# Optimization experiments

Measured on AMD Instinct MI355X. Metric: run time of the kernel, lower is better.

## Reference

```python
import jax, jax.numpy as jnp
import numpy as np
from jax import lax

# Model dims (mamba_ssm defaults: d_state=16, d_conv=4, expand=2, dt_rank=ceil(d_model/16))
V = 16384       # vocab_size
D = 1024        # embedding_dim / d_model
C_CLS = 128     # num_CLS_classes
D_INNER = 2 * D # expand * d_model = 2048
N = 16          # d_state
K = 4           # d_conv
DT_RANK = (D + 15) // 16  # 64
B, L = 4, 512


def setup_inputs() -> dict:
    key = jax.random.key(0)
    ks = jax.random.split(key, 12)
    s = 0.02
    tokens = jax.random.randint(ks[0], (B, L), 0, V, dtype=jnp.int64)
    embedding = jax.random.normal(ks[1], (V, D), jnp.float32) * s
    in_proj_w = jax.random.normal(ks[2], (2 * D_INNER, D), jnp.float32) * s
    conv_w = jax.random.normal(ks[3], (D_INNER, 1, K), jnp.float32) * 0.1
    conv_b = jnp.zeros((D_INNER,), jnp.float32)
    x_proj_w = jax.random.normal(ks[4], (DT_RANK + 2 * N, D_INNER), jnp.float32) * s
    dt_proj_w = jax.random.normal(ks[5], (D_INNER, DT_RANK), jnp.float32) * s
    dt_proj_b = jax.random.uniform(ks[6], (D_INNER,), jnp.float32, -4.0, -2.0)  # softplus -> small dt
    A_log = jnp.log(jnp.broadcast_to(jnp.arange(1, N + 1, dtype=jnp.float32), (D_INNER, N)))
    D_param = jnp.ones((D_INNER,), jnp.float32)
    out_proj_w = jax.random.normal(ks[7], (D, D_INNER), jnp.float32) * s
    recon_w = jax.random.normal(ks[8], (V, D), jnp.float32) * s
    cls_w = jax.random.normal(ks[9], (C_CLS, D), jnp.float32) * s
    return dict(tokens=tokens, embedding=embedding, in_proj_w=in_proj_w,
                conv_w=conv_w, conv_b=conv_b, x_proj_w=x_proj_w,
                dt_proj_w=dt_proj_w, dt_proj_b=dt_proj_b, A_log=A_log,
                D_param=D_param, out_proj_w=out_proj_w, recon_w=recon_w, cls_w=cls_w)


def _mamba(h, in_proj_w, conv_w, conv_b, x_proj_w, dt_proj_w, dt_proj_b, A_log, D_param, out_proj_w):
    # h: (B, L, D)
    xz = jnp.einsum('bld,ed->ble', h, in_proj_w)          # (B, L, 2*D_INNER)
    x, z = jnp.split(xz, 2, axis=-1)                      # each (B, L, D_INNER)
    # causal depthwise conv1d along L
    xt = jnp.swapaxes(x, 1, 2)                            # (B, D_INNER, L)
    xt = lax.conv_general_dilated(xt, conv_w, window_strides=(1,),
                                  padding=[(K - 1, 0)],
                                  feature_group_count=D_INNER,
                                  dimension_numbers=('NCH', 'OIH', 'NCH'))
    xt = xt + conv_b[None, :, None]
    x = jax.nn.silu(jnp.swapaxes(xt, 1, 2))               # (B, L, D_INNER)
    # input-dependent dt, B, C
    x_dbl = jnp.einsum('bld,ed->ble', x, x_proj_w)        # (B, L, DT_RANK+2N)
    dt, Bm, Cm = jnp.split(x_dbl, [DT_RANK, DT_RANK + N], axis=-1)
    delta = jax.nn.softplus(jnp.einsum('blr,dr->bld', dt, dt_proj_w) + dt_proj_b)  # (B,L,D_INNER)
    A = -jnp.exp(A_log)                                   # (D_INNER, N)
    dA = jnp.exp(delta[..., None] * A)                    # (B,L,D_INNER,N)
    dBx = delta[..., None] * Bm[:, :, None, :] * x[..., None]  # (B,L,D_INNER,N)
    # selective scan over time (sequential recurrence)
    dA_t = jnp.swapaxes(dA, 0, 1)                         # (L,B,D_INNER,N)
    dBx_t = jnp.swapaxes(dBx, 0, 1)
    C_t = jnp.swapaxes(Cm, 0, 1)                          # (L,B,N)
    def step(hc, inp):
        a, bx, c = inp
        hc = a * hc + bx                                  # (B,D_INNER,N)
        y = jnp.einsum('bdn,bn->bd', hc, c)
        return hc, y
    h0 = jnp.zeros((x.shape[0], D_INNER, N), x.dtype)
    _, ys = lax.scan(step, h0, (dA_t, dBx_t, C_t))
    y = jnp.swapaxes(ys, 0, 1) + x * D_param              # (B,L,D_INNER)
    y = y * jax.nn.silu(z)
    return jnp.einsum('ble,de->bld', y, out_proj_w)       # (B,L,D)


def reference(tokens, embedding, in_proj_w, conv_w, conv_b, x_proj_w,
              dt_proj_w, dt_proj_b, A_log, D_param, out_proj_w, recon_w, cls_w):
    h = embedding[tokens]                                 # (B,L,D)
    h = _mamba(h, in_proj_w, conv_w, conv_b, x_proj_w, dt_proj_w, dt_proj_b,
               A_log, D_param, out_proj_w)
    recon = jnp.einsum('bld,vd->blv', h, recon_w)         # (B,L,V)
    pooled = h.mean(axis=1)                               # mean CLS pooling assumption
    cls = jnp.einsum('bd,cd->bc', pooled, cls_w)          # (B,C_CLS)
    return (recon, cls)
```

## Files before the change

### kernel.cpp

```cpp
#include <hip/hip_runtime.h>
#include <hip/hip_bf16.h>
#include <stdint.h>

#define DIN    2048
#define MROWS  2048
#define LSEQ   512
#define NV     16384
#define DMODEL 1024
#define NC     8
#define CL     64

typedef __attribute__((ext_vector_type(8))) short bf16x8;
typedef __attribute__((ext_vector_type(4))) float f32x4;

__device__ __forceinline__ uint16_t f2bf(float f) {
  uint32_t u = __builtin_bit_cast(uint32_t, f);
  u += 0x7fffu + ((u >> 16) & 1u);
  return (uint16_t)(u >> 16);
}
__device__ __forceinline__ float bf2f(uint16_t u) {
  return __builtin_bit_cast(float, (uint32_t)u << 16);
}

__device__ __forceinline__ void gld_lds16(const uint16_t* g, uint16_t* l) {
  __builtin_amdgcn_global_load_lds(
      (const __attribute__((address_space(1))) void*)g,
      (__attribute__((address_space(3))) void*)l,
      16, 0, 0);
}

__global__ __launch_bounds__(512, 2) void gemm256_bf16_kernel(
    const uint16_t* __restrict__ A, const uint16_t* __restrict__ B,
    float* __restrict__ Cf, uint16_t* __restrict__ Cbf, int M, int N, int K)
{
  __shared__ uint16_t lds[4 * 16384];
  const int tid = threadIdx.x;
  const int w   = tid >> 6;
  const int l   = tid & 63;

  const int nwg = gridDim.x;
  const int cpx = nwg >> 3;
  const int swz = (blockIdx.x & 7) * cpx + (blockIdx.x >> 3);
  const int nmy = M >> 8;
  const int bm  = (swz % nmy) << 8;
  const int bn  = (swz / nmy) << 8;

  const int fr = l & 15;
  const int fg = l >> 4;
  const int wr = w >> 2;
  const int wc = w & 3;

  const int srow = l >> 2;
  const int kof  = (((l & 3) ^ ((l >> 3) & 3)) << 3);
  const int ar0  = (w * 2 + 0) * 16 + srow;
  const int ar1  = (w * 2 + 1) * 16 + srow;
  const uint16_t* Ag0 = A + (size_t)(bm + ar0) * K + kof;
  const uint16_t* Ag1 = A + (size_t)(bm + ar1) * K + kof;
  const uint16_t* Bg0 = B + (size_t)(bn + ar0) * K + kof;
  const uint16_t* Bg1 = B + (size_t)(bn + ar1) * K + kof;
  const int lA0 = (w * 2 + 0) * 512;
  const int lA1 = (w * 2 + 1) * 512;
  const int lB0 = 8192 + (w * 2 + 0) * 512;
  const int lB1 = 8192 + (w * 2 + 1) * 512;

  const int axr  = ((fg ^ ((fr >> 1) & 3)) << 3);
  const int aoff = (wr * 128 + fr) * 32 + axr;
  const int boff = 8192 + (wc * 64 + fr) * 32 + axr;

  f32x4 acc[8][4] = {};
  const int NT = K >> 5;

  auto stage_all = [&](int t) {
    const int sb = (t & 3) << 14;
    const int k0 = t << 5;
    gld_lds16(Ag0 + k0, lds + sb + lA0);
    gld_lds16(Ag1 + k0, lds + sb + lA1);
    gld_lds16(Bg0 + k0, lds + sb + lB0);
    gld_lds16(Bg1 + k0, lds + sb + lB1);
  };
  auto compute_full = [&](int sb) {
    bf16x8 af[8], bfr[4];
#pragma unroll
    for (int mi = 0; mi < 8; ++mi)
      af[mi] = *(const bf16x8*)(lds + sb + aoff + mi * 512);
#pragma unroll
    for (int ni = 0; ni < 4; ++ni)
      bfr[ni] = *(const bf16x8*)(lds + sb + boff + ni * 512);
    __builtin_amdgcn_s_setprio(1);
#pragma unroll
    for (int mi = 0; mi < 8; ++mi)
#pragma unroll
      for (int ni = 0; ni < 4; ++ni)
        acc[mi][ni] = __builtin_amdgcn_mfma_f32_16x16x32_bf16(af[mi], bfr[ni], acc[mi][ni], 0, 0, 0);
    __builtin_amdgcn_s_setprio(0);
  };

  stage_all(0); stage_all(1); stage_all(2);
  asm volatile("s_waitcnt vmcnt(8)" ::: "memory");
  __builtin_amdgcn_s_barrier();

  for (int t = 0; t < NT - 3; ++t) {
    const int sb = (t & 3) << 14;
    const int st = ((t + 3) & 3) << 14;
    const int k0 = (t + 3) << 5;
    bf16x8 af[8], bfr[4];
#pragma unroll
    for (int mi = 0; mi < 8; ++mi)
      af[mi] = *(const bf16x8*)(lds + sb + aoff + mi * 512);
    bfr[0] = *(const bf16x8*)(lds + sb + boff + 0 * 512);
    bfr[1] = *(const bf16x8*)(lds + sb + boff + 1 * 512);
    gld_lds16(Ag0 + k0, lds + st + lA0);
    gld_lds16(Ag1 + k0, lds + st + lA1);
    __builtin_amdgcn_s_barrier();
    asm volatile("s_waitcnt lgkmcnt(0)" ::: "memory");
    __builtin_amdgcn_sched_barrier(0);
    __builtin_amdgcn_s_setprio(1);
#pragma unroll
    for (int mi = 0; mi < 8; ++mi)
#pragma unroll
      for (int ni = 0; ni < 2; ++ni)
        acc[mi][ni] = __builtin_amdgcn_mfma_f32_16x16x32_bf16(af[mi], bfr[ni], acc[mi][ni], 0, 0, 0);
    __builtin_amdgcn_s_setprio(0);
    __builtin_amdgcn_s_barrier();
    bfr[2] = *(const bf16x8*)(lds + sb + boff + 2 * 512);
    bfr[3] = *(const bf16x8*)(lds + sb + boff + 3 * 512);
    gld_lds16(Bg0 + k0, lds + st + lB0);
    gld_lds16(Bg1 + k0, lds + st + lB1);
    __builtin_amdgcn_s_barrier();
    asm volatile("s_waitcnt lgkmcnt(0)" ::: "memory");
    __builtin_amdgcn_sched_barrier(0);
    __builtin_amdgcn_s_setprio(1);
#pragma unroll
    for (int mi = 0; mi < 8; ++mi)
#pragma unroll
      for (int ni = 2; ni < 4; ++ni)
        acc[mi][ni] = __builtin_amdgcn_mfma_f32_16x16x32_bf16(af[mi], bfr[ni], acc[mi][ni], 0, 0, 0);
    __builtin_amdgcn_s_setprio(0);
    asm volatile("s_waitcnt vmcnt(8)" ::: "memory");
    __builtin_amdgcn_s_barrier();
  }
  compute_full(((NT - 3) & 3) << 14);
  asm volatile("s_waitcnt vmcnt(4)" ::: "memory");
  __builtin_amdgcn_s_barrier();
  compute_full(((NT - 2) & 3) << 14);
  asm volatile("s_waitcnt vmcnt(0)" ::: "memory");
  __builtin_amdgcn_s_barrier();
  compute_full(((NT - 1) & 3) << 14);

#pragma unroll
  for (int mi = 0; mi < 8; ++mi) {
    const int r0 = bm + wr * 128 + mi * 16 + fg * 4;
#pragma unroll
    for (int ni = 0; ni < 4; ++ni) {
      const int c0 = bn + wc * 64 + ni * 16 + fr;
#pragma unroll
      for (int r = 0; r < 4; ++r) {
        const float v = acc[mi][ni][r];
        if (Cf)  Cf[(size_t)(r0 + r) * N + c0] = v;
        if (Cbf) Cbf[(size_t)(r0 + r) * N + c0] = f2bf(v);
      }
    }
  }
}

__global__ __launch_bounds__(256) void gemm_bf16_kernel(
    const uint16_t* __restrict__ A, const uint16_t* __restrict__ B,
    float* __restrict__ C, int M, int N, int K, int kchunk,
    const float* __restrict__ bias)
{
  __shared__ uint16_t As[128 * 32];
  __shared__ uint16_t Bs[128 * 32];
  const int tid  = threadIdx.x;
  const int wid  = tid >> 6;
  const int lane = tid & 63;
  const int bm = blockIdx.y * 128;
  const int bn = blockIdx.x * 128;
  const int k_beg = blockIdx.z * kchunk;
  float* Cout = C + (size_t)blockIdx.z * M * N;

  const int fr = lane & 15;
  const int fg = lane >> 4;
  const int wm = (wid >> 1) * 64;
  const int wn = (wid & 1) * 64;

  const int srow = wid * 32 + (lane >> 2);
  const int skof = (lane & 3) * 8;
  const uint16_t* Ag = A + (size_t)(bm + srow) * K + skof;
  const uint16_t* Bg = B + (size_t)(bn + srow) * K + skof;
  uint16_t* Al = As + wid * 1024;
  uint16_t* Bl = Bs + wid * 1024;

  f32x4 acc[4][4] = {};

  for (int k0 = 0; k0 < kchunk; k0 += 32) {
    const int kk = k_beg + k0;
    gld_lds16(Ag + kk, Al);
    gld_lds16(Ag + (size_t)16 * K + kk, Al + 512);
    gld_lds16(Bg + kk, Bl);
    gld_lds16(Bg + (size_t)16 * K + kk, Bl + 512);
    asm volatile("s_waitcnt vmcnt(0)" ::: "memory");
    __syncthreads();
    bf16x8 af[4], bfr[4];
#pragma unroll
    for (int i = 0; i < 4; ++i)
      af[i] = *(const bf16x8*)(As + (wm + i * 16 + fr) * 32 + fg * 8);
#pragma unroll
    for (int j = 0; j < 4; ++j)
      bfr[j] = *(const bf16x8*)(Bs + (wn + j * 16 + fr) * 32 + fg * 8);
#pragma unroll
    for (int i = 0; i < 4; ++i)
#pragma unroll
      for (int j = 0; j < 4; ++j)
        acc[i][j] = __builtin_amdgcn_mfma_f32_16x16x32_bf16(af[i], bfr[j], acc[i][j], 0, 0, 0);
    __syncthreads();
  }

#pragma unroll
  for (int i = 0; i < 4; ++i) {
    const int r0 = bm + wm + i * 16 + fg * 4;
#pragma unroll
    for (int j = 0; j < 4; ++j) {
      const int c0 = bn + wn + j * 16 + fr;
      const float bv = bias ? bias[c0] : 0.f;
#pragma unroll
      for (int r = 0; r < 4; ++r) {
        float v = acc[i][j][r];
        if (bias) {
          const float u = v + bv;
          v = (u > 20.f) ? u : log1pf(__expf(u));
        }
        Cout[(size_t)(r0 + r) * N + c0] = v;
      }
    }
  }
}

__global__ __launch_bounds__(256) void reduce4_dt_kernel(
    const float* __restrict__ in, float* __restrict__ xdbl, uint16_t* __restrict__ dtb) {
  const int i = blockIdx.x * 256 + threadIdx.x;
  const float s = in[i] + in[i + 262144] + in[i + 2 * 262144] + in[i + 3 * 262144];
  xdbl[i] = s;
  const int c = i & 127;
  if (c < 64) dtb[(i >> 7) * 64 + c] = f2bf(s);
}

__global__ __launch_bounds__(256) void reduce2_bf16_kernel(
    const float* __restrict__ in, uint16_t* __restrict__ outb, int n) {
  const int i = blockIdx.x * 256 + threadIdx.x;
  if (i >= n) return;
  outb[i] = f2bf(in[i] + in[i + (size_t)n]);
}

__global__ __launch_bounds__(256) void embed_kernel(
    const int* __restrict__ tok, const float* __restrict__ emb, uint16_t* __restrict__ out) {
  const int m = blockIdx.x;
  const int t = tok[m];
  const float4 v = ((const float4*)(emb + (size_t)t * DMODEL))[threadIdx.x];
  ((ushort4*)(out + (size_t)m * DMODEL))[threadIdx.x] =
      make_ushort4(f2bf(v.x), f2bf(v.y), f2bf(v.z), f2bf(v.w));
}

__global__ __launch_bounds__(256) void cvt_bf16_kernel(
    const float* __restrict__ in, uint16_t* __restrict__ out, int n4) {
  const int i = blockIdx.x * 256 + threadIdx.x;
  if (i >= n4) return;
  const float4 v = ((const float4*)in)[i];
  ((ushort4*)out)[i] = make_ushort4(f2bf(v.x), f2bf(v.y), f2bf(v.z), f2bf(v.w));
}

__global__ __launch_bounds__(256) void cvt_pad_kernel(
    const float* __restrict__ in, uint16_t* __restrict__ out, int rows_in, int cols4) {
  const int i = blockIdx.x * 256 + threadIdx.x;
  const int r = i / cols4, c = i % cols4;
  ushort4 o = make_ushort4(0, 0, 0, 0);
  if (r < rows_in) {
    const float4 v = ((const float4*)in)[(size_t)r * cols4 + c];
    o = make_ushort4(f2bf(v.x), f2bf(v.y), f2bf(v.z), f2bf(v.w));
  }
  ((ushort4*)out)[i] = o;
}

__global__ __launch_bounds__(256) void conv_silu_kernel(
    const float* __restrict__ xz, const float* __restrict__ cw, const float* __restrict__ cb,
    float* __restrict__ xc, uint16_t* __restrict__ xcb)
{
  const int idx = blockIdx.x * 256 + threadIdx.x;
  const int d = idx & (DIN - 1);
  const int m = idx >> 11;
  const int l = m & (LSEQ - 1);
  float acc = cb[d];
#pragma unroll
  for (int j = 0; j < 4; ++j) {
    const int lj = l - 3 + j;
    if (lj >= 0) acc += cw[d * 4 + j] * xz[(size_t)(m - 3 + j) * 4096 + d];
  }
  const float r = acc / (1.f + __expf(-acc));
  xc[idx] = r;
  xcb[idx] = f2bf(r);
}

__global__ __launch_bounds__(256) void scan_partial_kernel(
    const float* __restrict__ delta, const float* __restrict__ xc,
    const float* __restrict__ xdbl, const float* __restrict__ A_log,
    float* __restrict__ Pb, float* __restrict__ Qb)
{
  const int q = threadIdx.x & 3;
  const int d_idx = threadIdx.x >> 2;
  const int c = blockIdx.x;
  const int d = blockIdx.y * 64 + d_idx;
  const int b = blockIdx.z;
  float Arow[4];
#pragma unroll
  for (int n = 0; n < 4; ++n)
    Arow[n] = -expf(A_log[d * 16 + q * 4 + n]);
  float P[4] = {1.f, 1.f, 1.f, 1.f};
  float Q[4] = {0.f, 0.f, 0.f, 0.f};
  const int l0 = c * CL;
#pragma unroll 4
  for (int li = 0; li < CL; ++li) {
    const int m = b * LSEQ + l0 + li;
    const float de = delta[(size_t)m * DIN + d];
    const float xv = xc[(size_t)m * DIN + d];
    const float dx = de * xv;
    const float4 Bv = *(const float4*)(xdbl + (size_t)m * 128 + 64 + q * 4);
    const float bv[4] = {Bv.x, Bv.y, Bv.z, Bv.w};
#pragma unroll
    for (int n = 0; n < 4; ++n) {
      const float a = __expf(de * Arow[n]);
      P[n] *= a;
      Q[n] = a * Q[n] + dx * bv[n];
    }
  }
  const size_t o = ((size_t)(b * NC + c) * DIN + d) * 16 + q * 4;
  *(float4*)(Pb + o) = make_float4(P[0], P[1], P[2], P[3]);
  *(float4*)(Qb + o) = make_float4(Q[0], Q[1], Q[2], Q[3]);
}

__global__ __launch_bounds__(256) void scan_bounds_kernel(
    const float* __restrict__ Pb, const float* __restrict__ Qb, float* __restrict__ Hi)
{
  const int i = blockIdx.x * 256 + threadIdx.x;
  const int b = i >> 15;
  const int r = i & 32767;
  float h = 0.f;
#pragma unroll
  for (int c = 0; c < NC; ++c) {
    const size_t o = ((size_t)(b * NC + c) << 15) + r;
    Hi[o] = h;
    h = Pb[o] * h + Qb[o];
  }
}

__global__ __launch_bounds__(256) void scan_final_kernel(
    const float* __restrict__ delta, const float* __restrict__ xc,
    const float* __restrict__ xdbl, const float* __restrict__ xz,
    const float* __restrict__ A_log, const float* __restrict__ Dp,
    const float* __restrict__ Hi, uint16_t* __restrict__ yb)
{
  const int q = threadIdx.x & 3;
  const int d_idx = threadIdx.x >> 2;
  const int c = blockIdx.x;
  const int d = blockIdx.y * 64 + d_idx;
  const int b = blockIdx.z;
  float Arow[4];
#pragma unroll
  for (int n = 0; n < 4; ++n)
    Arow[n] = -expf(A_log[d * 16 + q * 4 + n]);
  const float dpd = Dp[d];
  const size_t o = ((size_t)(b * NC + c) * DIN + d) * 16 + q * 4;
  const float4 Hv = *(const float4*)(Hi + o);
  float h[4] = {Hv.x, Hv.y, Hv.z, Hv.w};
  const int l0 = c * CL;
#pragma unroll 2
  for (int li = 0; li < CL; ++li) {
    const int m = b * LSEQ + l0 + li;
    const float de = delta[(size_t)m * DIN + d];
    const float xv = xc[(size_t)m * DIN + d];
    const float dx = de * xv;
    const float4 Bv = *(const float4*)(xdbl + (size_t)m * 128 + 64 + q * 4);
    const float4 Cv = *(const float4*)(xdbl + (size_t)m * 128 + 80 + q * 4);
    const float bv[4] = {Bv.x, Bv.y, Bv.z, Bv.w};
    const float cv[4] = {Cv.x, Cv.y, Cv.z, Cv.w};
    float yp = 0.f;
#pragma unroll
    for (int n = 0; n < 4; ++n) {
      const float a = __expf(de * Arow[n]);
      h[n] = a * h[n] + dx * bv[n];
      yp += h[n] * cv[n];
    }
    yp += __shfl_xor(yp, 1);
    yp += __shfl_xor(yp, 2);
    if (q == 0) {
      const float z = xz[(size_t)m * 4096 + 2048 + d];
      const float sil = z / (1.f + __expf(-z));
      yb[(size_t)m * DIN + d] = f2bf((yp + xv * dpd) * sil);
    }
  }
}

__global__ __launch_bounds__(256) void pool1_kernel(
    const uint16_t* __restrict__ h2b, float* __restrict__ part) {
  const int b = blockIdx.x >> 4, s = blockIdx.x & 15;
  const int c = threadIdx.x * 4;
  const uint16_t* base = h2b + ((size_t)(b * LSEQ + s * 32)) * DMODEL + c;
  float a0 = 0, a1 = 0, a2 = 0, a3 = 0;
  for (int l = 0; l < 32; ++l) {
    const ushort4 v = *(const ushort4*)(base + (size_t)l * DMODEL);
    a0 += bf2f(v.x); a1 += bf2f(v.y); a2 += bf2f(v.z); a3 += bf2f(v.w);
  }
  *(float4*)(part + (size_t)blockIdx.x * DMODEL + c) = make_float4(a0, a1, a2, a3);
}

__global__ __launch_bounds__(256) void pool2_cls_kernel(
    const float* __restrict__ part, const float* __restrict__ w, float* __restrict__ out) {
  __shared__ float pl[DMODEL];
  const int b = blockIdx.x, t = threadIdx.x;
  float4 s = make_float4(0, 0, 0, 0);
  for (int k = 0; k < 16; ++k) {
    const float4 v = *(const float4*)(part + ((size_t)(b * 16 + k)) * DMODEL + t * 4);
    s.x += v.x; s.y += v.y; s.z += v.z; s.w += v.w;
  }
  const float inv = 1.f / (float)LSEQ;
  pl[t * 4 + 0] = s.x * inv; pl[t * 4 + 1] = s.y * inv;
  pl[t * 4 + 2] = s.z * inv; pl[t * 4 + 3] = s.w * inv;
  __syncthreads();
  if (t < 128) {
    const float* wr = w + (size_t)t * DMODEL;
    float acc = 0.f;
    for (int k = 0; k < DMODEL; ++k) acc += pl[k] * wr[k];
    out[b * 128 + t] = acc;
  }
}

extern "C" void kernel_launch(void* const* d_in, const int* in_sizes, int n_in,
                              void* d_out, int out_size, void* d_ws, size_t ws_size,
                              hipStream_t stream) {
  const int*   tokens    = (const int*)d_in[0];
  const float* embedding = (const float*)d_in[1];
  const float* in_proj_w = (const float*)d_in[2];
  const float* conv_w    = (const float*)d_in[3];
  const float* conv_b    = (const float*)d_in[4];
  const float* x_proj_w  = (const float*)d_in[5];
  const float* dt_proj_w = (const float*)d_in[6];
  const float* dt_proj_b = (const float*)d_in[7];
  const float* A_log     = (const float*)d_in[8];
  const float* D_param   = (const float*)d_in[9];
  const float* out_prj_w = (const float*)d_in[10];
  const float* recon_w   = (const float*)d_in[11];
  const float* cls_w     = (const float*)d_in[12];

  char* ws = (char*)d_ws;
  const size_t MB = 1024 * 1024;
  uint16_t* h_bf   = (uint16_t*)(ws + 0);
  uint16_t* w_in   = (uint16_t*)(ws + 4 * MB);
  float*    xz     = (float*)(ws + 12 * MB);
  float*    xc_f   = (float*)(ws + 44 * MB);
  uint16_t* xc_b   = (uint16_t*)(ws + 60 * MB);
  uint16_t* wx_bf  = (uint16_t*)(ws + 68 * MB);
  float*    xdbl   = (float*)(ws + 69 * MB);
  uint16_t* dt_bf  = (uint16_t*)(ws + 70 * MB);
  uint16_t* wdt_bf = (uint16_t*)(ws + 71 * MB);
  float*    delta  = (float*)(ws + 72 * MB);
  uint16_t* y_bf   = (uint16_t*)(ws + 88 * MB);
  uint16_t* h2_bf  = (uint16_t*)(ws + 96 * MB);
  float*    part   = (float*)(ws + 100 * MB);
  uint16_t* wout_bf = h_bf;
  uint16_t* wrec_bf = (uint16_t*)xz;
  float*    kscr    = delta;
  float*    Pbuf    = (float*)(ws + 60 * MB);
  float*    Qbuf    = (float*)(ws + 64 * MB);
  float*    Hinit   = (float*)(ws + 4 * MB);

  const int RECON = MROWS * NV;

  embed_kernel<<<dim3(MROWS), dim3(256), 0, stream>>>(tokens, embedding, h_bf);
  cvt_bf16_kernel<<<dim3(4096), dim3(256), 0, stream>>>(in_proj_w, w_in, 4096 * 1024 / 4);
  gemm256_bf16_kernel<<<dim3(128), dim3(512), 0, stream>>>(h_bf, w_in, xz, nullptr, MROWS, 4096, 1024);
  cvt_bf16_kernel<<<dim3(2048), dim3(256), 0, stream>>>(out_prj_w, wout_bf, 1024 * 2048 / 4);
  cvt_bf16_kernel<<<dim3(128), dim3(256), 0, stream>>>(dt_proj_w, wdt_bf, 2048 * 64 / 4);
  cvt_pad_kernel<<<dim3(256), dim3(256), 0, stream>>>(x_proj_w, wx_bf, 96, 512);
  conv_silu_kernel<<<dim3(16384), dim3(256), 0, stream>>>(xz, conv_w, conv_b, xc_f, xc_b);
  gemm_bf16_kernel<<<dim3(1, 16, 4), dim3(256), 0, stream>>>(xc_b, wx_bf, kscr, MROWS, 128, 2048, 512, nullptr);
  reduce4_dt_kernel<<<dim3(1024), dim3(256), 0, stream>>>(kscr, xdbl, dt_bf);
  gemm_bf16_kernel<<<dim3(16, 16, 1), dim3(256), 0, stream>>>(dt_bf, wdt_bf, delta, MROWS, DIN, 64, 64, dt_proj_b);
  scan_partial_kernel<<<dim3(NC, 32, 4), dim3(256), 0, stream>>>(delta, xc_f, xdbl, A_log, Pbuf, Qbuf);
  scan_bounds_kernel<<<dim3(512), dim3(256), 0, stream>>>(Pbuf, Qbuf, Hinit);
  scan_final_kernel<<<dim3(NC, 32, 4), dim3(256), 0, stream>>>(delta, xc_f, xdbl, xz, A_log, D_param, Hinit, y_bf);
  cvt_bf16_kernel<<<dim3(16384), dim3(256), 0, stream>>>(recon_w, wrec_bf, NV * 1024 / 4);
  gemm_bf16_kernel<<<dim3(8, 16, 2), dim3(256), 0, stream>>>(y_bf, wout_bf, kscr, MROWS, 1024, 2048, 1024, nullptr);
  reduce2_bf16_kernel<<<dim3(8192), dim3(256), 0, stream>>>(kscr, h2_bf, MROWS * 1024);
  gemm256_bf16_kernel<<<dim3(512), dim3(512), 0, stream>>>(h2_bf, wrec_bf, (float*)d_out, nullptr, MROWS, NV, 1024);
  pool1_kernel<<<dim3(64), dim3(256), 0, stream>>>(h2_bf, part);
  pool2_cls_kernel<<<dim3(4), dim3(256), 0, stream>>>(part, cls_w, (float*)d_out + RECON);
}
```

Measured before the change: 375.0 us.

## Rewrite 256x256 GEMM with BK=64 double-buffered 8-phase pipelined schedule

Replaces the four-stage BK=32 pipeline of the large bf16 GEMM with a two-buffer BK=64 scheme. Each K-tile is split into eight MFMA phases interleaved with LDS reads and global-to-LDS loads, using a new XOR swizzle for 128-byte rows. The aim is fewer barriers per unit of work and better overlap of loads with MFMA. The unused bf16 output path is dropped. The more complex phase schedule with many barriers risks stalls or occupancy changes.

```diff
diff --git a/kernel.cpp b/kernel.cpp
--- a/kernel.cpp
+++ b/kernel.cpp
@@ -29,11 +29,11 @@
       16, 0, 0);
 }
 
-__global__ __launch_bounds__(512, 2) void gemm256_bf16_kernel(
+__global__ __launch_bounds__(512, 2) void gemm256p8_kernel(
     const uint16_t* __restrict__ A, const uint16_t* __restrict__ B,
-    float* __restrict__ Cf, uint16_t* __restrict__ Cbf, int M, int N, int K)
-{
-  __shared__ uint16_t lds[4 * 16384];
+    float* __restrict__ C, int M, int N, int K)
+{
+  __shared__ uint16_t lds[2 * 32768];
   const int tid = threadIdx.x;
   const int w   = tid >> 6;
   const int l   = tid & 63;
@@ -50,102 +50,108 @@
   const int wr = w >> 2;
   const int wc = w & 3;
 
-  const int srow = l >> 2;
-  const int kof  = (((l & 3) ^ ((l >> 3) & 3)) << 3);
-  const int ar0  = (w * 2 + 0) * 16 + srow;
-  const int ar1  = (w * 2 + 1) * 16 + srow;
-  const uint16_t* Ag0 = A + (size_t)(bm + ar0) * K + kof;
-  const uint16_t* Ag1 = A + (size_t)(bm + ar1) * K + kof;
-  const uint16_t* Bg0 = B + (size_t)(bn + ar0) * K + kof;
-  const uint16_t* Bg1 = B + (size_t)(bn + ar1) * K + kof;
-  const int lA0 = (w * 2 + 0) * 512;
-  const int lA1 = (w * 2 + 1) * 512;
-  const int lB0 = 8192 + (w * 2 + 0) * 512;
-  const int lB1 = 8192 + (w * 2 + 1) * 512;
-
-  const int axr  = ((fg ^ ((fr >> 1) & 3)) << 3);
-  const int aoff = (wr * 128 + fr) * 32 + axr;
-  const int boff = 8192 + (wc * 64 + fr) * 32 + axr;
+  const int schunk = (l & 7) ^ (l >> 3);
+  const uint16_t* Ag = A + (size_t)(bm + w * 16 + (l >> 3)) * K + schunk * 8;
+  const uint16_t* Bg = B + (size_t)(bn + w * 16 + (l >> 3)) * K + schunk * 8;
+
+  const int ax0 = ((fg) ^ (fr & 7)) << 3;
+  const int ax1 = ((4 + fg) ^ (fr & 7)) << 3;
+  const int aA  = (wr * 128 + fr) * 64;
+  const int aB  = 16384 + (wc * 64 + fr) * 64;
 
   f32x4 acc[8][4] = {};
-  const int NT = K >> 5;
-
-  auto stage_all = [&](int t) {
-    const int sb = (t & 3) << 14;
-    const int k0 = t << 5;
-    gld_lds16(Ag0 + k0, lds + sb + lA0);
-    gld_lds16(Ag1 + k0, lds + sb + lA1);
-    gld_lds16(Bg0 + k0, lds + sb + lB0);
-    gld_lds16(Bg1 + k0, lds + sb + lB1);
+  bf16x8 af[4][2], b01[2][2], b23[2][2];
+
+  const int NT = K >> 6;
+  const int NITER = NT >> 1;
+
+  auto STG = [&](int t, int h) {
+    const uint16_t* g = ((h & 2) ? Bg : Ag) + ((h & 1) ? (size_t)128 * K : 0) + (size_t)t * 64;
+    uint16_t* d = lds + ((t & 1) << 15) + ((h & 2) << 13) + (((h & 1) << 7) + (w << 4)) * 64;
+    gld_lds16(g, d);
+    gld_lds16(g + (size_t)8 * K, d + 512);
   };
-  auto compute_full = [&](int sb) {
-    bf16x8 af[8], bfr[4];
-#pragma unroll
-    for (int mi = 0; mi < 8; ++mi)
-      af[mi] = *(const bf16x8*)(lds + sb + aoff + mi * 512);
-#pragma unroll
-    for (int ni = 0; ni < 4; ++ni)
-      bfr[ni] = *(const bf16x8*)(lds + sb + boff + ni * 512);
-    __builtin_amdgcn_s_setprio(1);
-#pragma unroll
-    for (int mi = 0; mi < 8; ++mi)
-#pragma unroll
-      for (int ni = 0; ni < 4; ++ni)
-        acc[mi][ni] = __builtin_amdgcn_mfma_f32_16x16x32_bf16(af[mi], bfr[ni], acc[mi][ni], 0, 0, 0);
-    __builtin_amdgcn_s_setprio(0);
-  };
-
-  stage_all(0); stage_all(1); stage_all(2);
-  asm volatile("s_waitcnt vmcnt(8)" ::: "memory");
-  __builtin_amdgcn_s_barrier();
-
-  for (int t = 0; t < NT - 3; ++t) {
-    const int sb = (t & 3) << 14;
-    const int st = ((t + 3) & 3) << 14;
-    const int k0 = (t + 3) << 5;
-    bf16x8 af[8], bfr[4];
-#pragma unroll
-    for (int mi = 0; mi < 8; ++mi)
-      af[mi] = *(const bf16x8*)(lds + sb + aoff + mi * 512);
-    bfr[0] = *(const bf16x8*)(lds + sb + boff + 0 * 512);
-    bfr[1] = *(const bf16x8*)(lds + sb + boff + 1 * 512);
-    gld_lds16(Ag0 + k0, lds + st + lA0);
-    gld_lds16(Ag1 + k0, lds + st + lA1);
-    __builtin_amdgcn_s_barrier();
-    asm volatile("s_waitcnt lgkmcnt(0)" ::: "memory");
-    __builtin_amdgcn_sched_barrier(0);
-    __builtin_amdgcn_s_setprio(1);
-#pragma unroll
-    for (int mi = 0; mi < 8; ++mi)
-#pragma unroll
-      for (int ni = 0; ni < 2; ++ni)
-        acc[mi][ni] = __builtin_amdgcn_mfma_f32_16x16x32_bf16(af[mi], bfr[ni], acc[mi][ni], 0, 0, 0);
-    __builtin_amdgcn_s_setprio(0);
-    __builtin_amdgcn_s_barrier();
-    bfr[2] = *(const bf16x8*)(lds + sb + boff + 2 * 512);
-    bfr[3] = *(const bf16x8*)(lds + sb + boff + 3 * 512);
-    gld_lds16(Bg0 + k0, lds + st + lB0);
-    gld_lds16(Bg1 + k0, lds + st + lB1);
-    __builtin_amdgcn_s_barrier();
-    asm volatile("s_waitcnt lgkmcnt(0)" ::: "memory");
-    __builtin_amdgcn_sched_barrier(0);
-    __builtin_amdgcn_s_setprio(1);
-#pragma unroll
-    for (int mi = 0; mi < 8; ++mi)
-#pragma unroll
-      for (int ni = 2; ni < 4; ++ni)
-        acc[mi][ni] = __builtin_amdgcn_mfma_f32_16x16x32_bf16(af[mi], bfr[ni], acc[mi][ni], 0, 0, 0);
-    __builtin_amdgcn_s_setprio(0);
-    asm volatile("s_waitcnt vmcnt(8)" ::: "memory");
-    __builtin_amdgcn_s_barrier();
-  }
-  compute_full(((NT - 3) & 3) << 14);
+
+#define LDSV(e) (*(const bf16x8*)(lds + (e)))
+#define RD_A(bo)                                                     \
+  _Pragma("unroll") for (int i = 0; i < 4; ++i) {                    \
+    af[i][0] = LDSV((bo) + aA + (mi0 + i) * 1024 + ax0);             \
+    af[i][1] = LDSV((bo) + aA + (mi0 + i) * 1024 + ax1); }
+#define RD_B(arr, ni0, bo)                                           \
+  _Pragma("unroll") for (int i = 0; i < 2; ++i) {                    \
+    arr[i][0] = LDSV((bo) + aB + ((ni0) + i) * 1024 + ax0);          \
+    arr[i][1] = LDSV((bo) + aB + ((ni0) + i) * 1024 + ax1); }
+#define BAR() __builtin_amdgcn_s_barrier()
+#define LGKM0() do { asm volatile("s_waitcnt lgkmcnt(0)" ::: "memory"); \
+                     __builtin_amdgcn_sched_barrier(0); } while (0)
+#define MFMA16(arr, mo, no)                                          \
+  do { __builtin_amdgcn_s_setprio(1);                                \
+    _Pragma("unroll") for (int mi = 0; mi < 4; ++mi)                 \
+    _Pragma("unroll") for (int ni = 0; ni < 2; ++ni)                 \
+    _Pragma("unroll") for (int kk = 0; kk < 2; ++kk)                 \
+      acc[(mo) + mi][(no) + ni] = __builtin_amdgcn_mfma_f32_16x16x32_bf16( \
+          af[mi][kk], arr[ni][kk], acc[(mo) + mi][(no) + ni], 0, 0, 0); \
+    __builtin_amdgcn_s_setprio(0); } while (0)
+
+  STG(0, 0); STG(0, 1); STG(0, 2); STG(0, 3); STG(1, 0); STG(1, 1);
   asm volatile("s_waitcnt vmcnt(4)" ::: "memory");
-  __builtin_amdgcn_s_barrier();
-  compute_full(((NT - 2) & 3) << 14);
-  asm volatile("s_waitcnt vmcnt(0)" ::: "memory");
-  __builtin_amdgcn_s_barrier();
-  compute_full(((NT - 1) & 3) << 14);
+  BAR();
+
+  for (int it = 0; it < NITER - 1; ++it) {
+    const int t = 2 * it;
+    int mi0;
+    mi0 = 0; RD_A(0); RD_B(b01, 0, 0);
+    STG(t + 1, 2);
+    BAR(); LGKM0(); MFMA16(b01, 0, 0); BAR();
+    RD_B(b23, 2, 0);
+    STG(t + 1, 3);
+    BAR(); LGKM0(); MFMA16(b23, 0, 2); BAR();
+    mi0 = 4; RD_A(0);
+    STG(t + 2, 0);
+    BAR(); LGKM0(); MFMA16(b01, 4, 0); BAR();
+    STG(t + 2, 1);
+    asm volatile("s_waitcnt vmcnt(4)" ::: "memory");
+    BAR(); MFMA16(b23, 4, 2); BAR();
+    mi0 = 0; RD_A(32768); RD_B(b01, 0, 32768);
+    STG(t + 2, 2);
+    BAR(); LGKM0(); MFMA16(b01, 0, 0); BAR();
+    RD_B(b23, 2, 32768);
+    STG(t + 2, 3);
+    BAR(); LGKM0(); MFMA16(b23, 0, 2); BAR();
+    mi0 = 4; RD_A(32768);
+    STG(t + 3, 0);
+    BAR(); LGKM0(); MFMA16(b01, 4, 0); BAR();
+    STG(t + 3, 1);
+    asm volatile("s_waitcnt vmcnt(4)" ::: "memory");
+    BAR(); MFMA16(b23, 4, 2); BAR();
+  }
+  {
+    const int t = NT - 2;
+    int mi0;
+    mi0 = 0; RD_A(0); RD_B(b01, 0, 0);
+    STG(t + 1, 2);
+    BAR(); LGKM0(); MFMA16(b01, 0, 0); BAR();
+    RD_B(b23, 2, 0);
+    STG(t + 1, 3);
+    BAR(); LGKM0(); MFMA16(b23, 0, 2); BAR();
+    mi0 = 4; RD_A(0);
+    BAR(); LGKM0(); MFMA16(b01, 4, 0); BAR();
+    asm volatile("s_waitcnt vmcnt(0)" ::: "memory");
+    BAR(); MFMA16(b23, 4, 2); BAR();
+    mi0 = 0; RD_A(32768); RD_B(b01, 0, 32768);
+    BAR(); LGKM0(); MFMA16(b01, 0, 0); BAR();
+    RD_B(b23, 2, 32768);
+    BAR(); LGKM0(); MFMA16(b23, 0, 2); BAR();
+    mi0 = 4; RD_A(32768);
+    BAR(); LGKM0(); MFMA16(b01, 4, 0); BAR();
+    MFMA16(b23, 4, 2);
+  }
+#undef LDSV
+#undef RD_A
+#undef RD_B
+#undef BAR
+#undef LGKM0
+#undef MFMA16
 
 #pragma unroll
   for (int mi = 0; mi < 8; ++mi) {
@@ -154,11 +160,8 @@
     for (int ni = 0; ni < 4; ++ni) {
       const int c0 = bn + wc * 64 + ni * 16 + fr;
 #pragma unroll
-      for (int r = 0; r < 4; ++r) {
-        const float v = acc[mi][ni][r];
-        if (Cf)  Cf[(size_t)(r0 + r) * N + c0] = v;
-        if (Cbf) Cbf[(size_t)(r0 + r) * N + c0] = f2bf(v);
-      }
+      for (int r = 0; r < 4; ++r)
+        C[(size_t)(r0 + r) * N + c0] = acc[mi][ni][r];
     }
   }
 }
@@ -475,7 +478,7 @@
 
   embed_kernel<<<dim3(MROWS), dim3(256), 0, stream>>>(tokens, embedding, h_bf);
   cvt_bf16_kernel<<<dim3(4096), dim3(256), 0, stream>>>(in_proj_w, w_in, 4096 * 1024 / 4);
-  gemm256_bf16_kernel<<<dim3(128), dim3(512), 0, stream>>>(h_bf, w_in, xz, nullptr, MROWS, 4096, 1024);
+  gemm256p8_kernel<<<dim3(128), dim3(512), 0, stream>>>(h_bf, w_in, xz, MROWS, 4096, 1024);
   cvt_bf16_kernel<<<dim3(2048), dim3(256), 0, stream>>>(out_prj_w, wout_bf, 1024 * 2048 / 4);
   cvt_bf16_kernel<<<dim3(128), dim3(256), 0, stream>>>(dt_proj_w, wdt_bf, 2048 * 64 / 4);
   cvt_pad_kernel<<<dim3(256), dim3(256), 0, stream>>>(x_proj_w, wx_bf, 96, 512);
@@ -489,7 +492,7 @@
   cvt_bf16_kernel<<<dim3(16384), dim3(256), 0, stream>>>(recon_w, wrec_bf, NV * 1024 / 4);
   gemm_bf16_kernel<<<dim3(8, 16, 2), dim3(256), 0, stream>>>(y_bf, wout_bf, kscr, MROWS, 1024, 2048, 1024, nullptr);
   reduce2_bf16_kernel<<<dim3(8192), dim3(256), 0, stream>>>(kscr, h2_bf, MROWS * 1024);
-  gemm256_bf16_kernel<<<dim3(512), dim3(512), 0, stream>>>(h2_bf, wrec_bf, (float*)d_out, nullptr, MROWS, NV, 1024);
+  gemm256p8_kernel<<<dim3(512), dim3(512), 0, stream>>>(h2_bf, wrec_bf, (float*)d_out, MROWS, NV, 1024);
   pool1_kernel<<<dim3(64), dim3(256), 0, stream>>>(h2_bf, part);
   pool2_cls_kernel<<<dim3(4), dim3(256), 0, stream>>>(part, cls_w, (float*)d_out + RECON);
 }
```

After: 387.5 us. +3.3%, slower.
